# Optimization experiments

Hardware: AMD Instinct MI355X
Metric: run time of the kernel (lower is better)

Reference implementation:

```python
import jax, jax.numpy as jnp
import numpy as np

NOTE_RES = 64  # global constant in the original repo; equals D of rep


def _down(x):
    # conv1d with kernel [0.5, 0.5], stride 2 over last axis (even length)
    return 0.5 * (x[..., ::2] + x[..., 1::2])


def setup_inputs() -> dict:
    key = jax.random.key(0)
    k1, k2, k3 = jax.random.split(key, 3)
    B, D, T = 32, NOTE_RES, 4096
    rep = jax.random.normal(k1, (B, D, T), dtype=jnp.float32)
    duration_mask = jax.random.uniform(k2, (B, D, T), dtype=jnp.float32)
    position_mask = jax.random.uniform(k3, (B, D, T), dtype=jnp.float32)
    return {
        "rep": rep,
        "duration_mask": duration_mask,
        "position_mask": position_mask,
        "low_duration": 1,
        "up_duration": 64,
    }


def reference(rep, duration_mask, position_mask, low_duration, up_duration):
    B, D, T = rep.shape  # D == NOTE_RES
    x = jnp.transpose(rep, (0, 2, 1))  # [B, T, NOTE_RES]; conv axis is last
    densed = _down(x)                  # [B, T, NOTE_RES//2]
    pot = NOTE_RES // 2
    res = jnp.zeros((B, T), dtype=rep.dtype)
    for i in range(0, NOTE_RES - low_duration):
        win_len = NOTE_RES - i - 1
        if win_len == pot:
            # descend one pyramid level
            x = densed
            densed = _down(x) if i < NOTE_RES - 2 else None
            d = x  # [B, T, win_len]
            pot //= 2
        else:
            pad_len = win_len - pot
            # mix fine-resolution prefix with coarse suffix -> length win_len
            d = jnp.concatenate([x[..., : 2 * pad_len], densed[..., pad_len:]], axis=-1)
        if win_len < up_duration:
            # sum_w d[b,t,w] * position_mask[b,w,t], gated by duration_mask[b,win_len-1,t]
            contrib = duration_mask[:, win_len - 1, :] * jnp.einsum(
                "btw,bwt->bt", d, position_mask[:, :win_len, :]
            )
            res = res + contrib
    return res[:, None, :]  # [B, 1, T]
```

## Files before the change

### kernel.cpp

```cpp
#include <hip/hip_runtime.h>


#define TT 4096

__device__ __forceinline__ void async_load16(const float* g, float* l) {
  __builtin_amdgcn_global_load_lds(
      (const __attribute__((address_space(1))) void*)g,
      (__attribute__((address_space(3))) void*)l, 16, 0, 0);
}

template <int P0, int P1>
__device__ __forceinline__ float role32(const float* __restrict__ lrep,
                                        const float* __restrict__ lpm,
                                        const float* __restrict__ ldm, int lane,
                                        int low, int up) {
  float xa[32 - P0];
#pragma unroll
  for (int k = P0; k < 32; ++k)
    xa[k - P0] = 0.5f * (lrep[(2 * k) * 64 + lane] + lrep[(2 * k + 1) * 64 + lane]);
  float q[P1 - 1];
#pragma unroll
  for (int j = 0; j < P1 - 1; ++j)
    q[j] = lrep[(2 * j) * 64 + lane] * lpm[(2 * j) * 64 + lane] +
           lrep[(2 * j + 1) * 64 + lane] * lpm[(2 * j + 1) * 64 + lane];
  float p = 0.f;
#pragma unroll
  for (int j = 0; j < P0; ++j) p += q[j];
  float res = 0.f;
#pragma unroll
  for (int pad = P0; pad < P1; ++pad) {
    const int L = 32 + pad;
    float s = p;
#pragma unroll
    for (int k = pad; k < 32; ++k)
      s = fmaf(xa[k - P0], lpm[(k + pad) * 64 + lane], s);
    if (L >= low && L < up)
      res = fmaf(ldm[(31 + pad) * 64 + lane], s, res);
    if (pad + 1 < P1) p += q[pad];
  }
  return res;
}

template <int M>
__device__ __forceinline__ void down_lds(const float* __restrict__ lpm, int lane,
                                         float* xa, float* q) {
#pragma unroll
  for (int j = 0; j < M; ++j) {
    const float a = xa[2 * j];
    const float c = xa[2 * j + 1];
    q[j] = a * lpm[(2 * j) * 64 + lane] + c * lpm[(2 * j + 1) * 64 + lane];
    xa[j] = 0.5f * (a + c);
  }
}

template <int M>
__device__ __forceinline__ void acc_lds(const float* __restrict__ lpm,
                                        const float* __restrict__ ldm, int lane,
                                        const float* xa, const float* q, int low,
                                        int up, float& res) {
  float p = 0.f;
#pragma unroll
  for (int pad = 0; pad < M; ++pad) {
    const int L = M + pad;
    float s = p;
#pragma unroll
    for (int k = pad; k < M; ++k) s = fmaf(xa[k], lpm[(k + pad) * 64 + lane], s);
    if (L >= low && L < up)
      res = fmaf(ldm[(M - 1 + pad) * 64 + lane], s, res);
    p += q[pad];
  }
}

__device__ __forceinline__ float role_tail(const float* __restrict__ lrep,
                                           const float* __restrict__ lpm,
                                           const float* __restrict__ ldm,
                                           int lane, int low, int up) {
  float xa[32];
#pragma unroll
  for (int k = 0; k < 32; ++k)
    xa[k] = 0.5f * (lrep[(2 * k) * 64 + lane] + lrep[(2 * k + 1) * 64 + lane]);
  float q[16];
  float res = 0.f;
  down_lds<16>(lpm, lane, xa, q);
  acc_lds<16>(lpm, ldm, lane, xa, q, low, up, res);
  down_lds<8>(lpm, lane, xa, q);
  acc_lds<8>(lpm, ldm, lane, xa, q, low, up, res);
  down_lds<4>(lpm, lane, xa, q);
  acc_lds<4>(lpm, ldm, lane, xa, q, low, up, res);
  down_lds<2>(lpm, lane, xa, q);
  acc_lds<2>(lpm, ldm, lane, xa, q, low, up, res);
  down_lds<1>(lpm, lane, xa, q);
  acc_lds<1>(lpm, ldm, lane, xa, q, low, up, res);
  return res;
}

__global__ __launch_bounds__(256, 3) void ContextGenerator_34875134444049_kernel(
    const float* __restrict__ rep, const float* __restrict__ dm,
    const float* __restrict__ pm, const int* __restrict__ lowp,
    const int* __restrict__ upp, float* __restrict__ out) {
  __shared__ float lds[192 * 64 + 192];
  const int wid = threadIdx.x >> 6;
  const int lane = threadIdx.x & 63;
  const int b = blockIdx.x >> 6;
  const int t0 = (blockIdx.x & 63) << 6;
  const size_t base = (size_t)b * 64 * TT + (size_t)t0;

  const size_t lv = (size_t)(lane >> 4) * TT + (size_t)((lane & 15) << 2);
  for (int g = wid; g < 48; g += 4) {
    const float* tbase = (g < 16) ? rep + base
                       : (g < 32) ? pm + base - (size_t)64 * TT
                                  : dm + base - (size_t)128 * TT;
    const float* src = tbase + (size_t)(g << 2) * TT + lv;
    async_load16(src, &lds[g * 256]);
  }

  const int low = lowp[0];
  const int up = upp[0];

  __syncthreads();

  const float* lrep = lds;
  const float* lpm = lds + 64 * 64;
  const float* ldm = lds + 128 * 64;
  float* part = lds + 192 * 64;

  float res;
  if (wid == 0)
    res = role32<0, 6>(lrep, lpm, ldm, lane, low, up);
  else if (wid == 1)
    res = role32<6, 13>(lrep, lpm, ldm, lane, low, up);
  else if (wid == 2)
    res = role32<13, 32>(lrep, lpm, ldm, lane, low, up);
  else
    res = role_tail(lrep, lpm, ldm, lane, low, up);

  if (wid < 3) part[wid * 64 + lane] = res;
  __syncthreads();
  if (wid == 3)
    out[(size_t)b * TT + t0 + lane] =
        res + part[lane] + part[64 + lane] + part[128 + lane];
}

extern "C" void kernel_launch(void* const* d_in, const int* in_sizes, int n_in,
                              void* d_out, int out_size, void* d_ws,
                              size_t ws_size, hipStream_t stream) {
  const float* rep = (const float*)d_in[0];
  const float* dm = (const float*)d_in[1];
  const float* pm = (const float*)d_in[2];
  const int* lowp = (const int*)d_in[3];
  const int* upp = (const int*)d_in[4];
  float* out = (float*)d_out;

  const int blocks = out_size / 64;
  ContextGenerator_34875134444049_kernel<<<blocks, 256, 0, stream>>>(
      rep, dm, pm, lowp, upp, out);
}
```

Measured before the change: 123.9 us.

## Split per-column work across six waves with rebalanced window roles

The block grows from four to six waves, and the window computations are regrouped into new roles. Three waves each cover an 8-wide slice of the coarse-level window sums. Another wave handles the first two pyramid levels, one runs the prefix-product accumulation, and one handles the deeper levels. Position-mask values are cached in registers rather than re-read from LDS, and the partial sums are reduced across six waves. The goal is to shorten the critical path of the slowest wave and raise parallelism, at the cost of more redundant downsampling work and higher register pressure.

```diff
diff --git a/kernel.cpp b/kernel.cpp
--- a/kernel.cpp
+++ b/kernel.cpp
@@ -9,96 +9,146 @@
       (__attribute__((address_space(3))) void*)l, 16, 0, 0);
 }
 
-template <int P0, int P1>
-__device__ __forceinline__ float role32(const float* __restrict__ lrep,
-                                        const float* __restrict__ lpm,
-                                        const float* __restrict__ ldm, int lane,
-                                        int low, int up) {
-  float xa[32 - P0];
-#pragma unroll
-  for (int k = P0; k < 32; ++k)
-    xa[k - P0] = 0.5f * (lrep[(2 * k) * 64 + lane] + lrep[(2 * k + 1) * 64 + lane]);
-  float q[P1 - 1];
-#pragma unroll
-  for (int j = 0; j < P1 - 1; ++j)
-    q[j] = lrep[(2 * j) * 64 + lane] * lpm[(2 * j) * 64 + lane] +
-           lrep[(2 * j + 1) * 64 + lane] * lpm[(2 * j + 1) * 64 + lane];
+template <int K0>
+__device__ __forceinline__ float roleK(const float* __restrict__ lrep,
+                                       const float* __restrict__ lpm,
+                                       const float* __restrict__ ldm, int lane,
+                                       int low, int up) {
+  constexpr int PADN = (K0 + 8 < 32) ? (K0 + 8) : 32;
+  constexpr int PMN = (2 * K0 + 14 < 62 ? 2 * K0 + 14 : 62) - K0 + 1;
+  float xa[8];
+#pragma unroll
+  for (int i = 0; i < 8; ++i)
+    xa[i] = 0.5f * (lrep[(2 * (K0 + i)) * 64 + lane] +
+                    lrep[(2 * (K0 + i) + 1) * 64 + lane]);
+  float pmv[PMN];
+#pragma unroll
+  for (int r = 0; r < PMN; ++r) pmv[r] = lpm[(K0 + r) * 64 + lane];
+  float res = 0.f;
+#pragma unroll
+  for (int pad = 0; pad < PADN; ++pad) {
+    const int L = 32 + pad;
+    const int kk0 = (pad > K0) ? pad : K0;
+    float s = 0.f;
+#pragma unroll
+    for (int k = kk0; k < K0 + 8; ++k)
+      s = fmaf(xa[k - K0], pmv[k + pad - K0], s);
+    if (L >= low && L < up) res = fmaf(ldm[(31 + pad) * 64 + lane], s, res);
+  }
+  return res;
+}
+
+__device__ __forceinline__ float role3(const float* __restrict__ lrep,
+                                       const float* __restrict__ lpm,
+                                       const float* __restrict__ ldm, int lane,
+                                       int low, int up) {
+  float pmv[31];
+#pragma unroll
+  for (int r = 0; r < 31; ++r) pmv[r] = lpm[r * 64 + lane];
+  float x1[32];
+#pragma unroll
+  for (int j = 0; j < 32; ++j)
+    x1[j] = 0.5f * (lrep[(2 * j) * 64 + lane] + lrep[(2 * j + 1) * 64 + lane]);
+  float res = 0.f;
+#pragma unroll
+  for (int pad = 0; pad < 8; ++pad) {
+    const int L = 32 + pad;
+    float s = 0.f;
+#pragma unroll
+    for (int k = pad; k < 8; ++k) s = fmaf(x1[k], pmv[k + pad], s);
+    if (L >= low && L < up) res = fmaf(ldm[(31 + pad) * 64 + lane], s, res);
+  }
+  float x2[16], q1[16];
+#pragma unroll
+  for (int j = 0; j < 16; ++j) {
+    const float a = x1[2 * j], b = x1[2 * j + 1];
+    x2[j] = 0.5f * (a + b);
+    q1[j] = a * pmv[2 * j] + b * pmv[2 * j + 1];
+  }
   float p = 0.f;
 #pragma unroll
-  for (int j = 0; j < P0; ++j) p += q[j];
-  float res = 0.f;
-#pragma unroll
-  for (int pad = P0; pad < P1; ++pad) {
+  for (int pad = 0; pad < 16; ++pad) {
+    const int L = 16 + pad;
+    float s = p;
+#pragma unroll
+    for (int k = pad; k < 16; ++k) s = fmaf(x2[k], pmv[k + pad], s);
+    if (L >= low && L < up) res = fmaf(ldm[(15 + pad) * 64 + lane], s, res);
+    p += q1[pad];
+  }
+  return res;
+}
+
+__device__ __forceinline__ float role4(const float* __restrict__ lrep,
+                                       const float* __restrict__ lpm,
+                                       const float* __restrict__ ldm, int lane,
+                                       int low, int up) {
+  float res = 0.f, p = 0.f;
+#pragma unroll
+  for (int pad = 1; pad < 32; ++pad) {
+    const int j = pad - 1;
+    const float a = lrep[(2 * j) * 64 + lane];
+    const float b = lrep[(2 * j + 1) * 64 + lane];
+    const float pa = lpm[(2 * j) * 64 + lane];
+    const float pb = lpm[(2 * j + 1) * 64 + lane];
+    p = fmaf(a, pa, fmaf(b, pb, p));
     const int L = 32 + pad;
-    float s = p;
-#pragma unroll
-    for (int k = pad; k < 32; ++k)
-      s = fmaf(xa[k - P0], lpm[(k + pad) * 64 + lane], s);
-    if (L >= low && L < up)
-      res = fmaf(ldm[(31 + pad) * 64 + lane], s, res);
-    if (pad + 1 < P1) p += q[pad];
+    if (L >= low && L < up) res = fmaf(ldm[(31 + pad) * 64 + lane], p, res);
   }
   return res;
 }
 
 template <int M>
-__device__ __forceinline__ void down_lds(const float* __restrict__ lpm, int lane,
-                                         float* xa, float* q) {
+__device__ __forceinline__ void level_step(const float* pmv,
+                                           const float* __restrict__ ldm,
+                                           int lane, int low, int up, float* xf,
+                                           float* xc, float& res) {
+  float q[M];
 #pragma unroll
   for (int j = 0; j < M; ++j) {
-    const float a = xa[2 * j];
-    const float c = xa[2 * j + 1];
-    q[j] = a * lpm[(2 * j) * 64 + lane] + c * lpm[(2 * j + 1) * 64 + lane];
-    xa[j] = 0.5f * (a + c);
-  }
-}
-
-template <int M>
-__device__ __forceinline__ void acc_lds(const float* __restrict__ lpm,
-                                        const float* __restrict__ ldm, int lane,
-                                        const float* xa, const float* q, int low,
-                                        int up, float& res) {
+    const float a = xf[2 * j], b = xf[2 * j + 1];
+    xc[j] = 0.5f * (a + b);
+    q[j] = a * pmv[2 * j] + b * pmv[2 * j + 1];
+  }
   float p = 0.f;
 #pragma unroll
   for (int pad = 0; pad < M; ++pad) {
     const int L = M + pad;
     float s = p;
 #pragma unroll
-    for (int k = pad; k < M; ++k) s = fmaf(xa[k], lpm[(k + pad) * 64 + lane], s);
-    if (L >= low && L < up)
-      res = fmaf(ldm[(M - 1 + pad) * 64 + lane], s, res);
+    for (int k = pad; k < M; ++k) s = fmaf(xc[k], pmv[k + pad], s);
+    if (L >= low && L < up) res = fmaf(ldm[(M - 1 + pad) * 64 + lane], s, res);
     p += q[pad];
   }
 }
 
-__device__ __forceinline__ float role_tail(const float* __restrict__ lrep,
-                                           const float* __restrict__ lpm,
-                                           const float* __restrict__ ldm,
-                                           int lane, int low, int up) {
-  float xa[32];
-#pragma unroll
-  for (int k = 0; k < 32; ++k)
-    xa[k] = 0.5f * (lrep[(2 * k) * 64 + lane] + lrep[(2 * k + 1) * 64 + lane]);
-  float q[16];
+__device__ __forceinline__ float role5(const float* __restrict__ lrep,
+                                       const float* __restrict__ lpm,
+                                       const float* __restrict__ ldm, int lane,
+                                       int low, int up) {
+  float pmv[15];
+#pragma unroll
+  for (int r = 0; r < 15; ++r) pmv[r] = lpm[r * 64 + lane];
+  float x1[32];
+#pragma unroll
+  for (int j = 0; j < 32; ++j)
+    x1[j] = 0.5f * (lrep[(2 * j) * 64 + lane] + lrep[(2 * j + 1) * 64 + lane]);
+  float x2[16];
+#pragma unroll
+  for (int j = 0; j < 16; ++j) x2[j] = 0.5f * (x1[2 * j] + x1[2 * j + 1]);
   float res = 0.f;
-  down_lds<16>(lpm, lane, xa, q);
-  acc_lds<16>(lpm, ldm, lane, xa, q, low, up, res);
-  down_lds<8>(lpm, lane, xa, q);
-  acc_lds<8>(lpm, ldm, lane, xa, q, low, up, res);
-  down_lds<4>(lpm, lane, xa, q);
-  acc_lds<4>(lpm, ldm, lane, xa, q, low, up, res);
-  down_lds<2>(lpm, lane, xa, q);
-  acc_lds<2>(lpm, ldm, lane, xa, q, low, up, res);
-  down_lds<1>(lpm, lane, xa, q);
-  acc_lds<1>(lpm, ldm, lane, xa, q, low, up, res);
-  return res;
-}
-
-__global__ __launch_bounds__(256, 3) void ContextGenerator_34875134444049_kernel(
+  float x3[8], x4[4], x5[2], x6[1];
+  level_step<8>(pmv, ldm, lane, low, up, x2, x3, res);
+  level_step<4>(pmv, ldm, lane, low, up, x3, x4, res);
+  level_step<2>(pmv, ldm, lane, low, up, x4, x5, res);
+  level_step<1>(pmv, ldm, lane, low, up, x5, x6, res);
+  return res;
+}
+
+__global__ __launch_bounds__(384, 3) void ContextGenerator_34875134444049_kernel(
     const float* __restrict__ rep, const float* __restrict__ dm,
     const float* __restrict__ pm, const int* __restrict__ lowp,
     const int* __restrict__ upp, float* __restrict__ out) {
-  __shared__ float lds[192 * 64 + 192];
+  __shared__ float lds[192 * 64 + 6 * 64];
   const int wid = threadIdx.x >> 6;
   const int lane = threadIdx.x & 63;
   const int b = blockIdx.x >> 6;
@@ -106,7 +156,7 @@
   const size_t base = (size_t)b * 64 * TT + (size_t)t0;
 
   const size_t lv = (size_t)(lane >> 4) * TT + (size_t)((lane & 15) << 2);
-  for (int g = wid; g < 48; g += 4) {
+  for (int g = wid; g < 48; g += 6) {
     const float* tbase = (g < 16) ? rep + base
                        : (g < 32) ? pm + base - (size_t)64 * TT
                                   : dm + base - (size_t)128 * TT;
@@ -126,19 +176,24 @@
 
   float res;
   if (wid == 0)
-    res = role32<0, 6>(lrep, lpm, ldm, lane, low, up);
+    res = roleK<24>(lrep, lpm, ldm, lane, low, up);
   else if (wid == 1)
-    res = role32<6, 13>(lrep, lpm, ldm, lane, low, up);
+    res = roleK<16>(lrep, lpm, ldm, lane, low, up);
   else if (wid == 2)
-    res = role32<13, 32>(lrep, lpm, ldm, lane, low, up);
+    res = roleK<8>(lrep, lpm, ldm, lane, low, up);
+  else if (wid == 3)
+    res = role3(lrep, lpm, ldm, lane, low, up);
+  else if (wid == 4)
+    res = role4(lrep, lpm, ldm, lane, low, up);
   else
-    res = role_tail(lrep, lpm, ldm, lane, low, up);
-
-  if (wid < 3) part[wid * 64 + lane] = res;
+    res = role5(lrep, lpm, ldm, lane, low, up);
+
+  if (wid > 0) part[wid * 64 + lane] = res;
   __syncthreads();
-  if (wid == 3)
-    out[(size_t)b * TT + t0 + lane] =
-        res + part[lane] + part[64 + lane] + part[128 + lane];
+  if (wid == 0)
+    out[(size_t)b * TT + t0 + lane] = res + part[64 + lane] + part[128 + lane] +
+                                      part[192 + lane] + part[256 + lane] +
+                                      part[320 + lane];
 }
 
 extern "C" void kernel_launch(void* const* d_in, const int* in_sizes, int n_in,
@@ -152,6 +207,6 @@
   float* out = (float*)d_out;
 
   const int blocks = out_size / 64;
-  ContextGenerator_34875134444049_kernel<<<blocks, 256, 0, stream>>>(
+  ContextGenerator_34875134444049_kernel<<<blocks, 384, 0, stream>>>(
       rep, dm, pm, lowp, upp, out);
 }
```

After: 125.7 us. Within noise of the previous version (+1.4%).
